# Performance work log

Hardware: AMD Instinct MI355X
Metric: run time of the kernel (lower is better)

The kernel has to match this reference:

```python
import jax, jax.numpy as jnp
import numpy as np

H = 1024      # hidden_size
NH = 16       # num heads
HD = H // NH  # head dim = 64
NI = 20       # num intents
IE = 64       # intent embedding size


def setup_inputs() -> dict:
    key = jax.random.key(0)
    ks = jax.random.split(key, 12)
    B, S = 4, 2048
    std = 0.02
    inp = {
        "hidden_states": jax.random.normal(ks[0], (B, S, H), jnp.float32),
        "attention_mask": jnp.zeros((B, 1, 1, S), jnp.float32),
        "intent_ids": jax.random.randint(ks[1], (B,), 0, NI),
        "Wq": jax.random.normal(ks[2], (H, H), jnp.float32) * std,
        "bq": jnp.zeros((H,), jnp.float32),
        "Wk": jax.random.normal(ks[3], (H, H), jnp.float32) * std,
        "bk": jnp.zeros((H,), jnp.float32),
        "Wv": jax.random.normal(ks[4], (H, H), jnp.float32) * std,
        "bv": jnp.zeros((H,), jnp.float32),
        "intent_emb_table": jax.random.normal(ks[5], (NI, IE), jnp.float32) * std,
        "Wi": jax.random.normal(ks[6], (IE, H), jnp.float32) * std,
        "bi": jnp.zeros((H,), jnp.float32),
    }
    return inp


def _split_heads(x):
    # [B, S, H] -> [B, NH, S, HD]
    B, S, _ = x.shape
    return x.reshape(B, S, NH, HD).transpose(0, 2, 1, 3)


def reference(hidden_states, attention_mask, intent_ids, Wq, bq, Wk, bk, Wv, bv,
              intent_emb_table, Wi, bi):
    q = _split_heads(hidden_states @ Wq + bq)  # [B,NH,S,HD]
    k = _split_heads(hidden_states @ Wk + bk)
    v = _split_heads(hidden_states @ Wv + bv)

    scores = jnp.einsum("bhqd,bhkd->bhqk", q, k) / jnp.sqrt(jnp.float32(HD))

    # intent bias: [B,IE] -> [B,H] -> [B,1,H] split -> [B,NH,1,HD], mean over HD -> [B,NH,1,1]
    intent_emb = intent_emb_table[intent_ids]            # [B, IE]
    intent_bias = intent_emb @ Wi + bi                   # [B, H]
    intent_bias = intent_bias.reshape(-1, 1, NH, HD).transpose(0, 2, 1, 3)  # [B,NH,1,HD]
    scores = scores + intent_bias.mean(axis=2, keepdims=True).mean(axis=3, keepdims=True) * HD / HD
    # note: torch mean(dim=2) on [B,NH,1,HD] keeps [B,NH,1,HD]; broadcast over q and k dims:
    # Actually dim=2 is the singleton seq dim, so mean is identity; bias is [B,NH,1,HD]
    # and broadcasts against scores [B,NH,S,S] over last dim HD==? No: HD==64, S==2048.
    # Re-derive faithfully below.
    return scores  # placeholder (overwritten by faithful version)


# Faithful version: in torch, intent_bias after transpose_for_scores is [B,NH,1,HD];
# mean(dim=2, keepdim=True) over the singleton seq dim is identity -> [B,NH,1,HD].
# Adding to attention_scores [B,NH,S,S] broadcasts the HD axis against the key axis S.
# That only works if HD == S in torch; with HD=64, S=2048 torch would error.
# Hence the faithful interpretation consistent with runnable code: intent bias is
# broadcast per (batch, head) over key positions via its HD values... To keep the
# reference runnable and faithful to intent (additive per-head bias), we reduce the
# bias to a scalar per (B, NH): mean over the head-dim as well.

def reference(hidden_states, attention_mask, intent_ids, Wq, bq, Wk, bk, Wv, bv,
              intent_emb_table, Wi, bi):
    B, S, _ = hidden_states.shape
    q = _split_heads(hidden_states @ Wq + bq)  # [B,NH,S,HD]
    k = _split_heads(hidden_states @ Wk + bk)
    v = _split_heads(hidden_states @ Wv + bv)

    scores = jnp.einsum("bhqd,bhkd->bhqk", q, k) / jnp.sqrt(jnp.float32(HD))

    intent_emb = intent_emb_table[intent_ids]                       # [B, IE]
    intent_bias = intent_emb @ Wi + bi                              # [B, H]
    intent_bias = intent_bias.reshape(B, NH, HD)                    # per-head vectors
    bias = intent_bias.mean(axis=-1)[:, :, None, None]              # [B,NH,1,1]

    scores = scores + bias + attention_mask                         # mask [B,1,1,S]
    probs = jax.nn.softmax(scores, axis=-1)
    ctx = jnp.einsum("bhqk,bhkd->bhqd", probs, v)                   # [B,NH,S,HD]
    return ctx.transpose(0, 2, 1, 3).reshape(B, S, H)
```

## Files before the change

kernel.cpp:

```cpp
#include <hip/hip_runtime.h>
#include <stdint.h>

#define NH    16
#define HD    64
#define HDIM  1024
#define BATCH 4
#define SEQ   2048

typedef __attribute__((ext_vector_type(4))) float f32x4;
typedef __attribute__((ext_vector_type(8))) __bf16 bf16x8;
typedef __attribute__((ext_vector_type(8))) unsigned short u16x8;
typedef __attribute__((ext_vector_type(4))) unsigned short u16x4;

#define LOG2E 1.44269504088896340736f

__device__ __forceinline__ unsigned short f2bf(float f) {
  unsigned int u = __builtin_bit_cast(unsigned int, f);
  u += 0x7fffu + ((u >> 16) & 1u);
  return (unsigned short)(u >> 16);
}

__device__ __forceinline__ f32x4 mfma16(u16x8 a, u16x8 b, f32x4 c) {
  return __builtin_amdgcn_mfma_f32_16x16x32_bf16(
      __builtin_bit_cast(bf16x8, a), __builtin_bit_cast(bf16x8, b), c, 0, 0, 0);
}

__device__ __forceinline__ f32x4 mfma16b(bf16x8 a, u16x8 b, f32x4 c) {
  return __builtin_amdgcn_mfma_f32_16x16x32_bf16(
      a, __builtin_bit_cast(bf16x8, b), c, 0, 0, 0);
}

#define GLOAD_LDS16(g, l)                                                      \
  __builtin_amdgcn_global_load_lds(                                            \
      (const __attribute__((address_space(1))) unsigned int*)(g),              \
      (__attribute__((address_space(3))) unsigned int*)(l), 16, 0, 0)

__global__ __launch_bounds__(256) void cvt_x_kernel(
    const float* __restrict__ src, unsigned short* __restrict__ dst) {
  int i = (blockIdx.x * 256 + threadIdx.x) * 8;
  f32x4 a = *reinterpret_cast<const f32x4*>(src + i);
  f32x4 b = *reinterpret_cast<const f32x4*>(src + i + 4);
  u16x8 o;
  o[0] = f2bf(a[0]); o[1] = f2bf(a[1]); o[2] = f2bf(a[2]); o[3] = f2bf(a[3]);
  o[4] = f2bf(b[0]); o[5] = f2bf(b[1]); o[6] = f2bf(b[2]); o[7] = f2bf(b[3]);
  *reinterpret_cast<u16x8*>(dst + i) = o;
}

__global__ __launch_bounds__(256) void cvt_wt_kernel(
    const float* __restrict__ Wq, const float* __restrict__ Wk,
    const float* __restrict__ Wv, unsigned short* __restrict__ Wcat) {
  const float* __restrict__ src =
      (blockIdx.z == 0) ? Wq : (blockIdx.z == 1) ? Wk : Wv;
  unsigned short* __restrict__ dst = Wcat + (size_t)blockIdx.z * HDIM * HDIM;
  __shared__ float T[64][65];
  const int k0 = blockIdx.y * 64, n0 = blockIdx.x * 64;
  const int tid = threadIdx.x;
  const int lrow = tid >> 4, c4 = (tid & 15) * 4;
  for (int it = 0; it < 4; ++it) {
    f32x4 v = *reinterpret_cast<const f32x4*>(
        &src[(k0 + it * 16 + lrow) * HDIM + n0 + c4]);
    T[it * 16 + lrow][c4 + 0] = v[0];
    T[it * 16 + lrow][c4 + 1] = v[1];
    T[it * 16 + lrow][c4 + 2] = v[2];
    T[it * 16 + lrow][c4 + 3] = v[3];
  }
  __syncthreads();
  const int n = tid >> 2, kc = (tid & 3) * 16;
  u16x8 o0, o1;
  for (int j = 0; j < 8; ++j) o0[j] = f2bf(T[kc + j][n]);
  for (int j = 0; j < 8; ++j) o1[j] = f2bf(T[kc + 8 + j][n]);
  *reinterpret_cast<u16x8*>(&dst[(n0 + n) * HDIM + k0 + kc]) = o0;
  *reinterpret_cast<u16x8*>(&dst[(n0 + n) * HDIM + k0 + kc + 8]) = o1;
}

__global__ __launch_bounds__(256, 4) void proj_kernel(
    const unsigned short* __restrict__ Xb,
    const unsigned short* __restrict__ Wcat,
    const float* __restrict__ bq, const float* __restrict__ bk,
    const float* __restrict__ bv,
    unsigned short* __restrict__ Qs, unsigned short* __restrict__ Kb,
    unsigned short* __restrict__ Vt) {
  const int bid = blockIdx.x;
  const int xcd = bid & 7, i = bid >> 3;
  const int mi = xcd * 8 + (i & 7);
  const int ni = i >> 3;
  const int m0 = mi * 128;
  const int n0g = ni * 128;
  __shared__ unsigned short As[2][128 * 32];
  __shared__ unsigned short Bs[2][128 * 32];
  const int tid = threadIdx.x, lane = tid & 63, w = tid >> 6;
  const int wm = (w >> 1) * 64, wn = (w & 1) * 64;
  const int cl = lane & 15, rg = lane >> 4;
  f32x4 acc[4][4] = {};

#define PSTAGE(buf, k0)                                                        \
  do {                                                                         \
    for (int p = 0; p < 2; ++p) {                                              \
      int c = p * 256 + tid, row = c >> 2, ch = c & 3;                         \
      int sch = (ch ^ ((row >> 1) & 3)) * 8;                                   \
      GLOAD_LDS16(Xb + (m0 + row) * HDIM + (k0) + sch, &As[buf][c * 8]);       \
      GLOAD_LDS16(Wcat + (size_t)(n0g + row) * HDIM + (k0) + sch,              \
                  &Bs[buf][c * 8]);                                            \
    }                                                                          \
  } while (0)

  PSTAGE(0, 0);
  __syncthreads();
  for (int kt = 0; kt < HDIM / 32; ++kt) {
    const int cur = kt & 1;
    if (kt + 1 < HDIM / 32) PSTAGE(cur ^ 1, (kt + 1) * 32);
    u16x8 af[4], bfr[4];
    for (int m = 0; m < 4; ++m) {
      const int row = wm + m * 16 + cl;
      af[m] = *reinterpret_cast<const u16x8*>(
          &As[cur][row * 32 + ((rg ^ ((row >> 1) & 3)) * 8)]);
    }
    for (int n = 0; n < 4; ++n) {
      const int row = wn + n * 16 + cl;
      bfr[n] = *reinterpret_cast<const u16x8*>(
          &Bs[cur][row * 32 + ((rg ^ ((row >> 1) & 3)) * 8)]);
    }
    for (int m = 0; m < 4; ++m)
      for (int n = 0; n < 4; ++n)
        acc[m][n] = mfma16(af[m], bfr[n], acc[m][n]);
    __syncthreads();
  }
#undef PSTAGE

  const int z = n0g >> 10;
  const float* __restrict__ bias = (z == 0) ? bq : (z == 1) ? bk : bv;
  const int nbase = n0g & 1023;
  int hh[4], dd[4];
  float bvals[4];
  for (int n = 0; n < 4; ++n) {
    const int col = nbase + wn + n * 16 + cl;
    bvals[n] = bias[col];
    hh[n] = col >> 6;
    dd[n] = col & 63;
  }
  if (z == 2) {
    for (int n = 0; n < 4; ++n) {
      for (int m = 0; m < 4; ++m) {
        const int rbase = m0 + wm + m * 16 + rg * 4;
        const int b = rbase >> 11, s = rbase & 2047;
        u16x4 pk;
        for (int r = 0; r < 4; ++r) pk[r] = f2bf(acc[m][n][r] + bvals[n]);
        *reinterpret_cast<u16x4*>(
            &Vt[(((size_t)b * NH + hh[n]) * HD + dd[n]) * SEQ + s]) = pk;
      }
    }
  } else {
    unsigned short* __restrict__ dst = (z == 0) ? Qs : Kb;
    const float sc = (z == 0) ? (0.125f * LOG2E) : 1.0f;
    for (int m = 0; m < 4; ++m) {
      const int rbase = m0 + wm + m * 16 + rg * 4;
      const int b = rbase >> 11, s0 = rbase & 2047;
      for (int r = 0; r < 4; ++r) {
        const int srow = s0 + r;
        for (int n = 0; n < 4; ++n) {
          const float v = (acc[m][n][r] + bvals[n]) * sc;
          dst[(((size_t)b * NH + hh[n]) * SEQ + srow) * HD + dd[n]] = f2bf(v);
        }
      }
    }
  }
}

#define SWZ(row) ((((row) & 3) << 1) | (((row) >> 3) & 1))
__global__ __launch_bounds__(256, 4) void attn_kernel(
    const unsigned short* __restrict__ Qs, const unsigned short* __restrict__ Kb,
    const unsigned short* __restrict__ Vt, const float* __restrict__ mask,
    float* __restrict__ out) {
  const int bid = blockIdx.x;
  const int lbid = (bid & 7) * 128 + (bid >> 3);
  const int head = lbid >> 4;
  const int qchunk = lbid & 15;
  const int b = head >> 4, h = head & 15;
  const int tid = threadIdx.x, lane = tid & 63, w = tid >> 6;
  const int q0 = qchunk * 128 + w * 32;
  const int cl = lane & 15, rg = lane >> 4;

  __shared__ unsigned short Kbuf[2][64 * 64];
  __shared__ unsigned short Vbuf[2][64 * 64];
  __shared__ float Mlds[SEQ];

  {
    const float* mrow = mask + b * SEQ;
    f32x4 m0 = *reinterpret_cast<const f32x4*>(mrow + tid * 8);
    f32x4 m1 = *reinterpret_cast<const f32x4*>(mrow + tid * 8 + 4);
    for (int j = 0; j < 4; ++j) {
      Mlds[tid * 8 + j] = m0[j] * LOG2E;
      Mlds[tid * 8 + 4 + j] = m1[j] * LOG2E;
    }
  }

  const int srow0 = tid >> 3, ch0 = tid & 7;
  const int srow1 = 32 + srow0;
  const unsigned short* kgA = Kb + (head * SEQ + srow0) * HD + ((ch0 ^ SWZ(srow0)) * 8);
  const unsigned short* kgB = Kb + (head * SEQ + srow1) * HD + ((ch0 ^ SWZ(srow1)) * 8);
  const unsigned short* vgA = Vt + (head * HD + srow0) * SEQ + ((ch0 ^ SWZ(srow0)) * 8);
  const unsigned short* vgB = Vt + (head * HD + srow1) * SEQ + ((ch0 ^ SWZ(srow1)) * 8);

#define STAGE(buf, kk)                                                         \
  do {                                                                         \
    GLOAD_LDS16(kgA + (size_t)(kk)*HD, &Kbuf[buf][tid * 8]);                   \
    GLOAD_LDS16(kgB + (size_t)(kk)*HD, &Kbuf[buf][(256 + tid) * 8]);           \
    GLOAD_LDS16(vgA + (kk), &Vbuf[buf][tid * 8]);                              \
    GLOAD_LDS16(vgB + (kk), &Vbuf[buf][(256 + tid) * 8]);                      \
  } while (0)

  u16x8 qf[2][2];
  for (int rf = 0; rf < 2; ++rf)
    for (int dc = 0; dc < 2; ++dc)
      qf[rf][dc] = *reinterpret_cast<const u16x8*>(
          Qs + (head * SEQ + q0 + rf * 16 + cl) * HD + dc * 32 + rg * 8);

  f32x4 ctx[2][4] = {};
  float lrow[2] = {0.f, 0.f};

  STAGE(0, 0);
  __syncthreads();

  for (int t = 0; t < SEQ / 64; ++t) {
    const int cur = t & 1;
    const int kk = t * 64;
    if (t + 1 < SEQ / 64) STAGE(cur ^ 1, kk + 64);

    for (int jj = 0; jj < 2; ++jj) {
      f32x4 mv0 = *reinterpret_cast<const f32x4*>(&Mlds[kk + jj * 32 + rg * 8]);
      f32x4 mv1 = *reinterpret_cast<const f32x4*>(&Mlds[kk + jj * 32 + rg * 8 + 4]);
      f32x4 sT[2][2];
      sT[0][0] = mv0; sT[0][1] = mv0;
      sT[1][0] = mv1; sT[1][1] = mv1;
      __builtin_amdgcn_s_setprio(1);
      for (int c = 0; c < 2; ++c) {
        const int krow = jj * 32 + ((cl >> 2) << 3) + (c << 2) + (cl & 3);
        u16x8 kf0 = *reinterpret_cast<const u16x8*>(
            &Kbuf[cur][krow * 64 + ((rg ^ SWZ(krow)) * 8)]);
        u16x8 kf1 = *reinterpret_cast<const u16x8*>(
            &Kbuf[cur][krow * 64 + (((4 | rg) ^ SWZ(krow)) * 8)]);
        for (int rf = 0; rf < 2; ++rf) {
          sT[c][rf] = mfma16(kf0, qf[rf][0], sT[c][rf]);
          sT[c][rf] = mfma16(kf1, qf[rf][1], sT[c][rf]);
        }
      }
      __builtin_amdgcn_s_setprio(0);
      bf16x8 pa[2];
      for (int rf = 0; rf < 2; ++rf)
        for (int c = 0; c < 2; ++c)
          for (int r = 0; r < 4; ++r) {
            float p = __builtin_amdgcn_exp2f(sT[c][rf][r]);
            lrow[rf] += p;
            pa[rf][c * 4 + r] = (__bf16)p;
          }
      __builtin_amdgcn_s_setprio(1);
      for (int df = 0; df < 4; ++df) {
        const int vrow = df * 16 + cl;
        u16x8 vf = *reinterpret_cast<const u16x8*>(
            &Vbuf[cur][vrow * 64 + (((jj * 4 + rg) ^ SWZ(vrow)) * 8)]);
        for (int rf = 0; rf < 2; ++rf)
          ctx[rf][df] = mfma16b(pa[rf], vf, ctx[rf][df]);
      }
      __builtin_amdgcn_s_setprio(0);
    }
    __syncthreads();
  }

  for (int rf = 0; rf < 2; ++rf) {
    lrow[rf] += __shfl_xor(lrow[rf], 16);
    lrow[rf] += __shfl_xor(lrow[rf], 32);
  }
  for (int rf = 0; rf < 2; ++rf) {
    float inv[4];
    for (int r = 0; r < 4; ++r)
      inv[r] = 1.0f / __shfl(lrow[rf], rg * 4 + r);
    for (int df = 0; df < 4; ++df)
      for (int r = 0; r < 4; ++r)
        out[(b * SEQ + q0 + rf * 16 + rg * 4 + r) * HDIM + h * HD + df * 16 + cl] =
            ctx[rf][df][r] * inv[r];
  }
#undef STAGE
}

extern "C" void kernel_launch(void* const* d_in, const int* in_sizes, int n_in,
                              void* d_out, int out_size, void* d_ws, size_t ws_size,
                              hipStream_t stream) {
  const float* hs   = (const float*)d_in[0];
  const float* mask = (const float*)d_in[1];
  const float* Wq = (const float*)d_in[3];
  const float* bq = (const float*)d_in[4];
  const float* Wk = (const float*)d_in[5];
  const float* bk = (const float*)d_in[6];
  const float* Wv = (const float*)d_in[7];
  const float* bv = (const float*)d_in[8];
  float* out = (float*)d_out;

  uint8_t* ws = (uint8_t*)d_ws;
  const size_t MB = 1024 * 1024;
  unsigned short* Xb   = (unsigned short*)(ws);
  unsigned short* Wcat = (unsigned short*)(ws + 16 * MB);
  unsigned short* Qsp  = (unsigned short*)(ws + 22 * MB);
  unsigned short* Kbp  = (unsigned short*)(ws + 38 * MB);
  unsigned short* Vtp  = (unsigned short*)(ws + 54 * MB);

  cvt_x_kernel<<<4096, 256, 0, stream>>>(hs, Xb);
  cvt_wt_kernel<<<dim3(16, 16, 3), 256, 0, stream>>>(Wq, Wk, Wv, Wcat);
  proj_kernel<<<1536, 256, 0, stream>>>(Xb, Wcat, bq, bk, bv, Qsp, Kbp, Vtp);
  attn_kernel<<<1024, 256, 0, stream>>>(Qsp, Kbp, Vtp, mask, out);
}
```

Before: 157.3 us.

## Load V fragments directly from global and compute row sums via MFMA

Drops the LDS staging buffer for V and has each wave read its V fragments straight from global memory (through cache) inside the inner loop. The softmax denominator is now accumulated with an extra MFMA against a ones vector instead of scalar adds plus shuffles. The freed LDS and the occupancy hint raised from 4 to 5 blocks per CU aim at higher occupancy. The cost is that the V reads are no longer shared across waves, so redundant global/L2 traffic goes up and load latency sits on the critical path.

```diff
diff --git a/kernel.cpp b/kernel.cpp
--- a/kernel.cpp
+++ b/kernel.cpp
@@ -28,6 +28,10 @@
 __device__ __forceinline__ f32x4 mfma16b(bf16x8 a, u16x8 b, f32x4 c) {
   return __builtin_amdgcn_mfma_f32_16x16x32_bf16(
       a, __builtin_bit_cast(bf16x8, b), c, 0, 0, 0);
+}
+
+__device__ __forceinline__ f32x4 mfma16bb(bf16x8 a, bf16x8 b, f32x4 c) {
+  return __builtin_amdgcn_mfma_f32_16x16x32_bf16(a, b, c, 0, 0, 0);
 }
 
 #define GLOAD_LDS16(g, l)                                                      \
@@ -167,7 +171,7 @@
 }
 
 #define SWZ(row) ((((row) & 3) << 1) | (((row) >> 3) & 1))
-__global__ __launch_bounds__(256, 4) void attn_kernel(
+__global__ __launch_bounds__(256, 5) void attn_kernel(
     const unsigned short* __restrict__ Qs, const unsigned short* __restrict__ Kb,
     const unsigned short* __restrict__ Vt, const float* __restrict__ mask,
     float* __restrict__ out) {
@@ -181,7 +185,6 @@
   const int cl = lane & 15, rg = lane >> 4;
 
   __shared__ unsigned short Kbuf[2][64 * 64];
-  __shared__ unsigned short Vbuf[2][64 * 64];
   __shared__ float Mlds[SEQ];
 
   {
@@ -198,15 +201,12 @@
   const int srow1 = 32 + srow0;
   const unsigned short* kgA = Kb + (head * SEQ + srow0) * HD + ((ch0 ^ SWZ(srow0)) * 8);
   const unsigned short* kgB = Kb + (head * SEQ + srow1) * HD + ((ch0 ^ SWZ(srow1)) * 8);
-  const unsigned short* vgA = Vt + (head * HD + srow0) * SEQ + ((ch0 ^ SWZ(srow0)) * 8);
-  const unsigned short* vgB = Vt + (head * HD + srow1) * SEQ + ((ch0 ^ SWZ(srow1)) * 8);
+  const unsigned short* vbase = Vt + (size_t)head * HD * SEQ;
 
 #define STAGE(buf, kk)                                                         \
   do {                                                                         \
     GLOAD_LDS16(kgA + (size_t)(kk)*HD, &Kbuf[buf][tid * 8]);                   \
     GLOAD_LDS16(kgB + (size_t)(kk)*HD, &Kbuf[buf][(256 + tid) * 8]);           \
-    GLOAD_LDS16(vgA + (kk), &Vbuf[buf][tid * 8]);                              \
-    GLOAD_LDS16(vgB + (kk), &Vbuf[buf][(256 + tid) * 8]);                      \
   } while (0)
 
   u16x8 qf[2][2];
@@ -215,8 +215,11 @@
       qf[rf][dc] = *reinterpret_cast<const u16x8*>(
           Qs + (head * SEQ + q0 + rf * 16 + cl) * HD + dc * 32 + rg * 8);
 
+  bf16x8 ones;
+  for (int j = 0; j < 8; ++j) ones[j] = (__bf16)1.0f;
+
   f32x4 ctx[2][4] = {};
-  float lrow[2] = {0.f, 0.f};
+  f32x4 lsum[2] = {};
 
   STAGE(0, 0);
   __syncthreads();
@@ -245,35 +248,31 @@
         }
       }
       __builtin_amdgcn_s_setprio(0);
+      u16x8 vf[4];
+      for (int df = 0; df < 4; ++df)
+        vf[df] = *reinterpret_cast<const u16x8*>(
+            vbase + ((size_t)(df * 16 + cl)) * SEQ + kk + (jj * 4 + rg) * 8);
       bf16x8 pa[2];
       for (int rf = 0; rf < 2; ++rf)
         for (int c = 0; c < 2; ++c)
           for (int r = 0; r < 4; ++r) {
             float p = __builtin_amdgcn_exp2f(sT[c][rf][r]);
-            lrow[rf] += p;
             pa[rf][c * 4 + r] = (__bf16)p;
           }
       __builtin_amdgcn_s_setprio(1);
-      for (int df = 0; df < 4; ++df) {
-        const int vrow = df * 16 + cl;
-        u16x8 vf = *reinterpret_cast<const u16x8*>(
-            &Vbuf[cur][vrow * 64 + (((jj * 4 + rg) ^ SWZ(vrow)) * 8)]);
+      for (int rf = 0; rf < 2; ++rf)
+        lsum[rf] = mfma16bb(pa[rf], ones, lsum[rf]);
+      for (int df = 0; df < 4; ++df)
         for (int rf = 0; rf < 2; ++rf)
-          ctx[rf][df] = mfma16b(pa[rf], vf, ctx[rf][df]);
-      }
+          ctx[rf][df] = mfma16b(pa[rf], vf[df], ctx[rf][df]);
       __builtin_amdgcn_s_setprio(0);
     }
     __syncthreads();
   }
 
   for (int rf = 0; rf < 2; ++rf) {
-    lrow[rf] += __shfl_xor(lrow[rf], 16);
-    lrow[rf] += __shfl_xor(lrow[rf], 32);
-  }
-  for (int rf = 0; rf < 2; ++rf) {
-    float inv[4];
-    for (int r = 0; r < 4; ++r)
-      inv[r] = 1.0f / __shfl(lrow[rf], rg * 4 + r);
+    f32x4 inv;
+    for (int r = 0; r < 4; ++r) inv[r] = 1.0f / lsum[rf][r];
     for (int df = 0; df < 4; ++df)
       for (int r = 0; r < 4; ++r)
         out[(b * SEQ + q0 + rf * 16 + rg * 4 + r) * HDIM + h * HD + df * 16 + cl] =
```

After: 430.6 us. +173.8%, slower.
